# Kernel tuning notes

Hardware: AMD Instinct MI355X
Metric: run time of the kernel (lower is better)

The kernel has to match this reference:

```python
import jax, jax.numpy as jnp
import numpy as np


def _safe_pow(v, p):
    # mimic torch.nan_to_num(pow(v, p), nan=0, posinf=0, neginf=0) for v >= 0
    out = jnp.where(v > 0, jnp.power(jnp.where(v > 0, v, 1.0), p), 0.0)
    return out.astype(jnp.float32)


def setup_inputs() -> dict:
    key = jax.random.key(0)
    k1, k2, k3 = jax.random.split(key, 3)
    N, E, Din, Dout = 20000, 4096, 128, 128
    x = jax.random.normal(k1, (N, Din), dtype=jnp.float32)
    H = jax.random.uniform(k2, (N, E), dtype=jnp.float32)
    W = jax.random.normal(k3, (Dout, Din), dtype=jnp.float32) * (1.0 / np.sqrt(Din))
    b = jnp.zeros((Dout,), dtype=jnp.float32)
    return {"x": x, "H": H, "W": W, "b": b}


def reference(x, H, W, b):
    # Dv^{-1/2}: node degrees; De^{-1}: hyperedge degrees.
    # torch.diag(...)**p with nan/inf->0 is exactly diagonal scaling, so we
    # use broadcasted vector scaling fused around the two GEMMs.
    dv = _safe_pow(jnp.sum(H, axis=-1), -0.5)   # [N]
    de = _safe_pow(jnp.sum(H, axis=0), -1.0)    # [E]
    x = dv[:, None] * x                          # Dv^{-1/2} x
    x = H.T @ x                                  # [E, Din]
    x = de[:, None] * x                          # De^{-1}
    x = H @ x                                    # [N, Din]
    x = dv[:, None] * x                          # Dv^{-1/2}
    return x @ W.T + b                           # Linear
```

## Files before the change

kernel.cpp:

```cpp
#include <hip/hip_runtime.h>
#include <hip/hip_bf16.h>
#include <stdint.h>


#define N_ 20000
#define E_ 4096
#define D_ 128
#define XTB_S 20032
#define SPLIT 12

typedef __attribute__((ext_vector_type(8))) short    bf16x8;
typedef __attribute__((ext_vector_type(4))) float    f32x4;
typedef __attribute__((ext_vector_type(8))) unsigned short us8;
typedef __attribute__((ext_vector_type(4))) unsigned short us4;

__device__ __forceinline__ unsigned short f2bf(float f) {
  unsigned u = __float_as_uint(f);
  u += 0x7FFFu + ((u >> 16) & 1u);
  return (unsigned short)(u >> 16);
}
__device__ __forceinline__ unsigned cvtpk(float lo, float hi) {
  unsigned r;
  asm("v_cvt_pk_bf16_f32 %0, %1, %2" : "=v"(r) : "v"(lo), "v"(hi));
  return r;
}
__device__ __forceinline__ void gload16(const unsigned short* g, unsigned short* l) {
  __builtin_amdgcn_global_load_lds(
      (const __attribute__((address_space(1))) unsigned int*)g,
      (__attribute__((address_space(3))) unsigned int*)l, 16, 0, 0);
}

__global__ __launch_bounds__(256) void k_pre(const float* __restrict__ H,
                                             const float* __restrict__ x,
                                             const float* __restrict__ W,
                                             float* __restrict__ dv,
                                             unsigned short* __restrict__ Hb,
                                             unsigned short* __restrict__ xTb,
                                             unsigned short* __restrict__ Wb) {
  const int t = threadIdx.x, lane = t & 63, w = t >> 6;
  const int b = blockIdx.x;
  if (b >= 2500) {
    const size_t base = (size_t)(20000 + (b - 2500) * 8) * E_;
    for (int i = t; i < 4096; i += 256)
      *(us8*)&Hb[base + (size_t)i * 8] = (us8){0,0,0,0,0,0,0,0};
    if (b == 2500 && t < 128) {
#pragma unroll
      for (int c = 0; c < 4; ++c)
        *(us8*)&xTb[(size_t)t * XTB_S + 20000 + c * 8] = (us8){0,0,0,0,0,0,0,0};
    }
    if (b == 2501) {
      int base2 = t * 64;
#pragma unroll
      for (int i = 0; i < 8; ++i) {
        const float* wp = W + base2 + i * 8;
        f32x4 a = *(const f32x4*)wp, b4 = *(const f32x4*)(wp + 4);
        union { us8 v; unsigned u[4]; } un;
        un.u[0] = cvtpk(a.x, a.y);   un.u[1] = cvtpk(a.z, a.w);
        un.u[2] = cvtpk(b4.x, b4.y); un.u[3] = cvtpk(b4.z, b4.w);
        *(us8*)(Wb + base2 + i * 8) = un.v;
      }
    }
    return;
  }
  __shared__ float red[32];
  __shared__ float xt[8 * 128];
  const int n0 = b * 8;
  { int r = t >> 5, d4 = (t & 31) * 4;
    *(f32x4*)&xt[r * 128 + d4] = *(const f32x4*)(x + (size_t)(n0 + r) * D_ + d4); }
  float rs[8];
#pragma unroll
  for (int r = 0; r < 8; ++r) {
    rs[r] = 0.f;
    const float* rp = H + (size_t)(n0 + r) * E_;
    unsigned short* hp = Hb + (size_t)(n0 + r) * E_;
#pragma unroll
    for (int j = 0; j < 4; ++j) {
      f32x4 v = *(const f32x4*)(rp + j * 1024 + t * 4);
      rs[r] += (v.x + v.y) + (v.z + v.w);
      union { us4 v4; unsigned u32[2]; } un;
      un.u32[0] = cvtpk(v.x, v.y);
      un.u32[1] = cvtpk(v.z, v.w);
      *(us4*)(hp + j * 1024 + t * 4) = un.v4;
    }
  }
#pragma unroll
  for (int r = 0; r < 8; ++r)
#pragma unroll
    for (int off = 32; off; off >>= 1) rs[r] += __shfl_xor(rs[r], off);
  if (lane == 0) {
#pragma unroll
    for (int r = 0; r < 8; ++r) red[w * 8 + r] = rs[r];
  }
  __syncthreads();
  if (t < 8) {
    float s = red[t] + red[8 + t] + red[16 + t] + red[24 + t];
    float d = s > 0.f ? rsqrtf(s) : 0.f;
    dv[n0 + t] = d;
    red[t] = d;
  }
  __syncthreads();
  if (t < 128) {
    int d = t;
    float v[8];
#pragma unroll
    for (int r = 0; r < 8; ++r) v[r] = xt[r * 128 + d] * red[r];
    union { us8 v8; unsigned u32[4]; } un;
#pragma unroll
    for (int j = 0; j < 4; ++j) un.u32[j] = cvtpk(v[2 * j], v[2 * j + 1]);
    *(us8*)(xTb + (size_t)d * XTB_S + n0) = un.v8;
  }
}

__global__ __launch_bounds__(256) void k_gemm1(const unsigned short* __restrict__ Hb,
                                               const unsigned short* __restrict__ xTb,
                                               float* __restrict__ partialT,
                                               float* __restrict__ desumP) {
  __shared__ unsigned short lH[2][64 * 64];
  __shared__ unsigned short lX[2][128 * 64];
  const int t = threadIdx.x, lane = t & 63, w = t >> 6;
  const int virt = (blockIdx.x & 7) * 96 + (blockIdx.x >> 3);
  const int eb = virt & 63, s = virt >> 6;
  const int e0 = eb * 64;
  const int g0 = (s * 313) / SPLIT;
  const int g1 = ((s + 1) * 313) / SPLIT;
  const int lrow = lane >> 3, lslot = lane & 7;
  const int bswz = (lslot ^ lrow) << 3;
  const int wy = w >> 1, wx = w & 1;
  const int ep = t & 31, q = t >> 5;
  const int er0 = 2 * ep, er1 = 2 * ep + 1;
  const int sl0 = (q ^ (er0 & 7)) << 3, sl1 = (q ^ (er1 & 7)) << 3;

  f32x4 acc[4][2];
  f32x4 accC[2];
#pragma unroll
  for (int i = 0; i < 4; ++i)
#pragma unroll
    for (int j = 0; j < 2; ++j) acc[i][j] = (f32x4){0.f, 0.f, 0.f, 0.f};
  accC[0] = (f32x4){0.f, 0.f, 0.f, 0.f};
  accC[1] = (f32x4){0.f, 0.f, 0.f, 0.f};
  bf16x8 ones;
#pragma unroll
  for (int i = 0; i < 8; ++i) ones[i] = (short)0x3F80;

  unsigned hr[8];
  auto LOADH = [&](int g) {
    const unsigned short* p = Hb + (size_t)(g * 64 + q * 8) * E_ + e0 + er0;
#pragma unroll
    for (int j = 0; j < 8; ++j) hr[j] = *(const unsigned*)(p + (size_t)j * E_);
  };
  auto WRITEH = [&](int bufi) {
    union { bf16x8 v; unsigned u[4]; } lo, hi;
#pragma unroll
    for (int p = 0; p < 4; ++p) {
      lo.u[p] = (hr[2 * p] & 0xFFFFu) | (hr[2 * p + 1] << 16);
      hi.u[p] = (hr[2 * p] >> 16) | (hr[2 * p + 1] & 0xFFFF0000u);
    }
    *(bf16x8*)&lH[bufi][er0 * 64 + sl0] = lo.v;
    *(bf16x8*)&lH[bufi][er1 * 64 + sl1] = hi.v;
  };
  auto GLOADX = [&](int g, int bufi) {
#pragma unroll
    for (int i = 0; i < 4; ++i) {
      int c = w * 4 + i;
      gload16(xTb + (size_t)(8 * c + lrow) * XTB_S + g * 64 + bswz,
              &lX[bufi][c * 512]);
    }
  };

  LOADH(g0); GLOADX(g0, 0); WRITEH(0);
  __syncthreads();
  int cur = 0;
  for (int it = g0; it < g1; ++it) {
    bool hn = it + 1 < g1;
    if (hn) { LOADH(it + 1); GLOADX(it + 1, cur ^ 1); }
    const int kg = lane >> 4, fr = lane & 15;
    bf16x8 ax[4][2], bh[2][2];
#pragma unroll
    for (int mi = 0; mi < 4; ++mi) {
      int m = wy * 64 + mi * 16 + fr;
#pragma unroll
      for (int kk = 0; kk < 2; ++kk)
        ax[mi][kk] = *(const bf16x8*)&lX[cur][m * 64 + (((kk * 4 + kg) ^ (m & 7)) << 3)];
    }
#pragma unroll
    for (int ni = 0; ni < 2; ++ni) {
      int n = wx * 32 + ni * 16 + fr;
#pragma unroll
      for (int kk = 0; kk < 2; ++kk)
        bh[ni][kk] = *(const bf16x8*)&lH[cur][n * 64 + (((kk * 4 + kg) ^ (n & 7)) << 3)];
    }
#pragma unroll
    for (int kk = 0; kk < 2; ++kk)
#pragma unroll
      for (int mi = 0; mi < 4; ++mi)
#pragma unroll
        for (int ni = 0; ni < 2; ++ni)
          acc[mi][ni] = __builtin_amdgcn_mfma_f32_16x16x32_bf16(ax[mi][kk], bh[ni][kk], acc[mi][ni], 0, 0, 0);
    if (wy == 0) {
#pragma unroll
      for (int kk = 0; kk < 2; ++kk)
#pragma unroll
        for (int ni = 0; ni < 2; ++ni)
          accC[ni] = __builtin_amdgcn_mfma_f32_16x16x32_bf16(ones, bh[ni][kk], accC[ni], 0, 0, 0);
    }
    if (hn) WRITEH(cur ^ 1);
    __syncthreads();
    cur ^= 1;
  }
  const int kg = lane >> 4, fr = lane & 15;
  if (wy == 0 && kg == 0) {
#pragma unroll
    for (int ni = 0; ni < 2; ++ni)
      desumP[s * E_ + e0 + wx * 32 + ni * 16 + fr] = accC[ni][0];
  }
#pragma unroll
  for (int mi = 0; mi < 4; ++mi)
#pragma unroll
    for (int ni = 0; ni < 2; ++ni)
#pragma unroll
      for (int r = 0; r < 4; ++r) {
        int d = wy * 64 + mi * 16 + kg * 4 + r;
        int e = e0 + wx * 32 + ni * 16 + fr;
        partialT[((size_t)s * 128 + d) * E_ + e] = acc[mi][ni][r];
      }
}

__global__ __launch_bounds__(256) void k_mid(const float* __restrict__ partialT,
                                             const float* __restrict__ desumP,
                                             const unsigned short* __restrict__ Wb,
                                             unsigned short* __restrict__ x3WT) {
  __shared__ unsigned short lW[128 * 136];
  __shared__ unsigned short lE[16 * 132];
  __shared__ float lT[128 * 20];
  const int t = threadIdx.x, lane = t & 63, w = t >> 6;
  const int e0 = blockIdx.x * 16;

  {
    int j = t >> 1, half = (t & 1) * 64;
    const us8* src = (const us8*)(Wb + (size_t)j * 128 + half);
#pragma unroll
    for (int i = 0; i < 8; ++i)
      *(us8*)&lW[j * 136 + half + 8 * i] = src[i];
  }
  {
    const int e = e0 + (t & 15);
    const int d0 = (t >> 4) * 8;
    float des = 0.f;
#pragma unroll
    for (int s = 0; s < SPLIT; ++s) des += desumP[s * E_ + e];
    float dei = des > 0.f ? 1.f / des : 0.f;
    float accp[8];
#pragma unroll
    for (int i = 0; i < 8; ++i) accp[i] = 0.f;
#pragma unroll
    for (int s = 0; s < SPLIT; ++s) {
      const float* p = partialT + ((size_t)s * 128 + d0) * E_ + e;
#pragma unroll
      for (int i = 0; i < 8; ++i) accp[i] += p[(size_t)i * E_];
    }
    union { bf16x8 v; unsigned u[4]; } un;
#pragma unroll
    for (int i = 0; i < 4; ++i)
      un.u[i] = cvtpk(accp[2 * i] * dei, accp[2 * i + 1] * dei);
    *(bf16x8*)&lE[(t & 15) * 132 + d0] = un.v;
  }
  __syncthreads();
  const int kg = lane >> 4, fr = lane & 15;
  f32x4 acc[2];
  acc[0] = (f32x4){0.f, 0.f, 0.f, 0.f};
  acc[1] = (f32x4){0.f, 0.f, 0.f, 0.f};
#pragma unroll
  for (int kk = 0; kk < 4; ++kk) {
    bf16x8 bfrag = *(const bf16x8*)&lE[fr * 132 + (kk * 4 + kg) * 8];
#pragma unroll
    for (int mi = 0; mi < 2; ++mi) {
      int m = w * 32 + mi * 16 + fr;
      bf16x8 afrag = *(const bf16x8*)&lW[m * 136 + (kk * 4 + kg) * 8];
      acc[mi] = __builtin_amdgcn_mfma_f32_16x16x32_bf16(afrag, bfrag, acc[mi], 0, 0, 0);
    }
  }
  __syncthreads();
#pragma unroll
  for (int mi = 0; mi < 2; ++mi)
#pragma unroll
    for (int r = 0; r < 4; ++r)
      lT[(w * 32 + mi * 16 + kg * 4 + r) * 20 + fr] = acc[mi][r];
  __syncthreads();
  {
    int j = t >> 1, eh = (t & 1) * 8;
    float v[8];
#pragma unroll
    for (int i = 0; i < 8; ++i) v[i] = lT[j * 20 + eh + i];
    union { us8 v8; unsigned u[4]; } un;
#pragma unroll
    for (int i = 0; i < 4; ++i) un.u[i] = cvtpk(v[2 * i], v[2 * i + 1]);
    *(us8*)(x3WT + (size_t)j * E_ + e0 + eh) = un.v8;
  }
}

__global__ __launch_bounds__(256) void k_gemm2(const unsigned short* __restrict__ Hb,
                                               const unsigned short* __restrict__ x3WT,
                                               float* __restrict__ P) {
  __shared__ unsigned short lA[2][64 * 64];
  __shared__ unsigned short lB[2][128 * 64];
  const int t = threadIdx.x, lane = t & 63, w = t >> 6;
  const int tile = blockIdx.x >> 1, half = blockIdx.x & 1;
  const int n0b = tile * 64;
  const int gbase = half * 32;
  const int lrow = lane >> 3, lslot = lane & 7;
  const int bswz = (lslot ^ lrow) << 3;
  const int wy = w >> 1, wx = w & 1;

  auto GLOADA = [&](int g, int bufi) {
#pragma unroll
    for (int i = 0; i < 2; ++i) {
      int c = w * 2 + i;
      gload16(Hb + (size_t)(n0b + 8 * c + lrow) * E_ + g * 64 + bswz,
              &lA[bufi][c * 512]);
    }
  };
  auto GLOADB = [&](int g, int bufi) {
#pragma unroll
    for (int i = 0; i < 4; ++i) {
      int c = w * 4 + i;
      gload16(x3WT + (size_t)(8 * c + lrow) * E_ + g * 64 + bswz,
              &lB[bufi][c * 512]);
    }
  };

  f32x4 acc[2][4];
#pragma unroll
  for (int i = 0; i < 2; ++i)
#pragma unroll
    for (int j = 0; j < 4; ++j) acc[i][j] = (f32x4){0.f, 0.f, 0.f, 0.f};

  GLOADA(gbase, 0); GLOADB(gbase, 0);
  __syncthreads();
  int cur = 0;
  for (int it = 0; it < 32; ++it) {
    bool hn = it < 31;
    if (hn) { GLOADA(gbase + it + 1, cur ^ 1); GLOADB(gbase + it + 1, cur ^ 1); }
    const int kg = lane >> 4, fr = lane & 15;
    bf16x8 af[2][2], bfr[4][2];
#pragma unroll
    for (int mi = 0; mi < 2; ++mi) {
      int m = wy * 32 + mi * 16 + fr;
#pragma unroll
      for (int kk = 0; kk < 2; ++kk)
        af[mi][kk] = *(const bf16x8*)&lA[cur][m * 64 + (((kk * 4 + kg) ^ (m & 7)) << 3)];
    }
#pragma unroll
    for (int ni = 0; ni < 4; ++ni) {
      int d = wx * 64 + ni * 16 + fr;
#pragma unroll
      for (int kk = 0; kk < 2; ++kk)
        bfr[ni][kk] = *(const bf16x8*)&lB[cur][d * 64 + (((kk * 4 + kg) ^ (d & 7)) << 3)];
    }
#pragma unroll
    for (int kk = 0; kk < 2; ++kk)
#pragma unroll
      for (int mi = 0; mi < 2; ++mi)
#pragma unroll
        for (int ni = 0; ni < 4; ++ni)
          acc[mi][ni] = __builtin_amdgcn_mfma_f32_16x16x32_bf16(af[mi][kk], bfr[ni][kk], acc[mi][ni], 0, 0, 0);
    __syncthreads();
    cur ^= 1;
  }
  const int kg = lane >> 4, fr = lane & 15;
  float* Ph = P + (size_t)half * N_ * D_;
#pragma unroll
  for (int mi = 0; mi < 2; ++mi)
#pragma unroll
    for (int ni = 0; ni < 4; ++ni) {
      int j2 = wx * 64 + ni * 16 + fr;
#pragma unroll
      for (int r = 0; r < 4; ++r) {
        int n = n0b + wy * 32 + mi * 16 + kg * 4 + r;
        if (n < N_) Ph[(size_t)n * D_ + j2] = acc[mi][ni][r];
      }
    }
}

__global__ __launch_bounds__(256) void k_out(const float* __restrict__ P,
                                             const float* __restrict__ dv,
                                             const float* __restrict__ bias,
                                             float* __restrict__ out) {
  int tid = blockIdx.x * 256 + threadIdx.x;
  int n = tid >> 4, jb = (tid & 15) * 8;
  size_t off = (size_t)n * D_ + jb;
  f32x4 p0a = *(const f32x4*)(P + off);
  f32x4 p0b = *(const f32x4*)(P + off + 4);
  f32x4 p1a = *(const f32x4*)(P + (size_t)N_ * D_ + off);
  f32x4 p1b = *(const f32x4*)(P + (size_t)N_ * D_ + off + 4);
  f32x4 ba  = *(const f32x4*)(bias + jb);
  f32x4 bb  = *(const f32x4*)(bias + jb + 4);
  float d = dv[n];
  f32x4 oa = (p0a + p1a) * d + ba;
  f32x4 ob = (p0b + p1b) * d + bb;
  *(f32x4*)(out + off)     = oa;
  *(f32x4*)(out + off + 4) = ob;
}

extern "C" void kernel_launch(void* const* d_in, const int* in_sizes, int n_in,
                              void* d_out, int out_size, void* d_ws, size_t ws_size,
                              hipStream_t stream) {
  const float* x = (const float*)d_in[0];
  const float* H = (const float*)d_in[1];
  const float* W = (const float*)d_in[2];
  const float* b = (const float*)d_in[3];
  float* out = (float*)d_out;
  char* ws = (char*)d_ws;
  float*          desumP   = (float*)(ws);
  float*          dv       = (float*)(ws + 196608);
  unsigned short* Wb       = (unsigned short*)(ws + 276736);
  unsigned short* xTb      = (unsigned short*)(ws + 309504);
  unsigned short* x3WT     = (unsigned short*)(ws + 5437696);
  float*          partialT = (float*)(ws + 6486272);
  unsigned short* Hb       = (unsigned short*)(ws + 31652096);
  float*          P        = (float*)(ws + 195754240);

  k_pre<<<2504, 256, 0, stream>>>(H, x, W, dv, Hb, xTb, Wb);
  k_gemm1<<<768, 256, 0, stream>>>(Hb, xTb, partialT, desumP);
  k_mid<<<256, 256, 0, stream>>>(partialT, desumP, Wb, x3WT);
  k_gemm2<<<626, 256, 0, stream>>>(Hb, x3WT, P);
  k_out<<<1250, 256, 0, stream>>>(P, dv, b, out);
}
```

Baseline: 213.7 us.

## Deepen H register prefetch to two stages with explicit waitcnt and barriers

Turns the first GEMM's main loop into a two-stage register pipeline for H tiles. Two register sets alternate so the global load for tile it+2 is issued while tile it+1 is written to LDS and tile it is computed. The __syncthreads calls are replaced by explicit vmcnt/lgkmcnt waits and raw barriers, and the MFMA block is wrapped in s_setprio, all to hide global load latency behind compute. In exchange it uses more registers and relies on hand-counted waitcnt values that must match the number of outstanding loads.

```diff
diff --git a/kernel.cpp b/kernel.cpp
--- a/kernel.cpp
+++ b/kernel.cpp
@@ -29,6 +29,9 @@
       (const __attribute__((address_space(1))) unsigned int*)g,
       (__attribute__((address_space(3))) unsigned int*)l, 16, 0, 0);
 }
+#define VMCNT(n) asm volatile("s_waitcnt vmcnt(" #n ")" ::: "memory")
+#define LGKM0()  asm volatile("s_waitcnt lgkmcnt(0)" ::: "memory")
+#define BAR()    do { __builtin_amdgcn_s_barrier(); __builtin_amdgcn_sched_barrier(0); } while (0)
 
 __global__ __launch_bounds__(256) void k_pre(const float* __restrict__ H,
                                              const float* __restrict__ x,
@@ -142,13 +145,13 @@
 #pragma unroll
   for (int i = 0; i < 8; ++i) ones[i] = (short)0x3F80;
 
-  unsigned hr[8];
-  auto LOADH = [&](int g) {
+  unsigned hrA[8], hrB[8];
+  auto LOADH = [&](int g, unsigned (&hr)[8]) {
     const unsigned short* p = Hb + (size_t)(g * 64 + q * 8) * E_ + e0 + er0;
 #pragma unroll
     for (int j = 0; j < 8; ++j) hr[j] = *(const unsigned*)(p + (size_t)j * E_);
   };
-  auto WRITEH = [&](int bufi) {
+  auto WRITEH = [&](unsigned (&hr)[8], int bufi) {
     union { bf16x8 v; unsigned u[4]; } lo, hi;
 #pragma unroll
     for (int p = 0; p < 4; ++p) {
@@ -167,12 +170,10 @@
     }
   };
 
-  LOADH(g0); GLOADX(g0, 0); WRITEH(0);
-  __syncthreads();
-  int cur = 0;
-  for (int it = g0; it < g1; ++it) {
-    bool hn = it + 1 < g1;
-    if (hn) { LOADH(it + 1); GLOADX(it + 1, cur ^ 1); }
+  auto STEP = [&](int it, unsigned (&ld)[8], unsigned (&wr)[8], int par) {
+    const bool hn = it + 1 < g1;
+    if (hn) GLOADX(it + 1, par ^ 1);
+    { int g2 = (it + 2 < g1) ? it + 2 : g1 - 1; LOADH(g2, ld); }
     const int kg = lane >> 4, fr = lane & 15;
     bf16x8 ax[4][2], bh[2][2];
 #pragma unroll
@@ -180,15 +181,16 @@
       int m = wy * 64 + mi * 16 + fr;
 #pragma unroll
       for (int kk = 0; kk < 2; ++kk)
-        ax[mi][kk] = *(const bf16x8*)&lX[cur][m * 64 + (((kk * 4 + kg) ^ (m & 7)) << 3)];
+        ax[mi][kk] = *(const bf16x8*)&lX[par][m * 64 + (((kk * 4 + kg) ^ (m & 7)) << 3)];
     }
 #pragma unroll
     for (int ni = 0; ni < 2; ++ni) {
       int n = wx * 32 + ni * 16 + fr;
 #pragma unroll
       for (int kk = 0; kk < 2; ++kk)
-        bh[ni][kk] = *(const bf16x8*)&lH[cur][n * 64 + (((kk * 4 + kg) ^ (n & 7)) << 3)];
-    }
+        bh[ni][kk] = *(const bf16x8*)&lH[par][n * 64 + (((kk * 4 + kg) ^ (n & 7)) << 3)];
+    }
+    __builtin_amdgcn_s_setprio(1);
 #pragma unroll
     for (int kk = 0; kk < 2; ++kk)
 #pragma unroll
@@ -203,10 +205,28 @@
         for (int ni = 0; ni < 2; ++ni)
           accC[ni] = __builtin_amdgcn_mfma_f32_16x16x32_bf16(ones, bh[ni][kk], accC[ni], 0, 0, 0);
     }
-    if (hn) WRITEH(cur ^ 1);
-    __syncthreads();
-    cur ^= 1;
-  }
+    __builtin_amdgcn_s_setprio(0);
+    __builtin_amdgcn_sched_barrier(0);
+    if (hn) WRITEH(wr, par ^ 1);
+    VMCNT(8);
+    LGKM0();
+    BAR();
+  };
+
+  LOADH(g0, hrA);
+  GLOADX(g0, 0);
+  LOADH(g0 + 1, hrB);
+  WRITEH(hrA, 0);
+  VMCNT(8);
+  LGKM0();
+  BAR();
+
+  int it = g0;
+  while (it < g1) {
+    STEP(it, hrA, hrB, 0); ++it;
+    if (it < g1) { STEP(it, hrB, hrA, 1); ++it; }
+  }
+
   const int kg = lane >> 4, fr = lane & 15;
   if (wy == 0 && kg == 0) {
 #pragma unroll
```

After: 224.5 us. 1.05x slower.

## Drop LDS staging in gemm2; load MFMA fragments directly from global memory

Applied to the files above, without the earlier changes.

Rewrites the second GEMM kernel so each wave computes a 16-row by 128-column tile and reads its A and B MFMA fragments straight from global memory, removing the LDS double buffer and the block-wide barriers. The goal is to cut LDS traffic and synchronisation overhead. In exchange, B (x3WT) is re-read from global/L2 by every wave with no sharing through LDS. Per-lane 16-byte loads are strided across rows, which may give poorer coalescing and more pressure on L2 bandwidth.

```diff
diff --git a/kernel.cpp b/kernel.cpp
--- a/kernel.cpp
+++ b/kernel.cpp
@@ -301,84 +301,40 @@
 __global__ __launch_bounds__(256) void k_gemm2(const unsigned short* __restrict__ Hb,
                                                const unsigned short* __restrict__ x3WT,
                                                float* __restrict__ P) {
-  __shared__ unsigned short lA[2][64 * 64];
-  __shared__ unsigned short lB[2][128 * 64];
   const int t = threadIdx.x, lane = t & 63, w = t >> 6;
   const int tile = blockIdx.x >> 1, half = blockIdx.x & 1;
-  const int n0b = tile * 64;
-  const int gbase = half * 32;
-  const int lrow = lane >> 3, lslot = lane & 7;
-  const int bswz = (lslot ^ lrow) << 3;
-  const int wy = w >> 1, wx = w & 1;
-
-  auto GLOADA = [&](int g, int bufi) {
-#pragma unroll
-    for (int i = 0; i < 2; ++i) {
-      int c = w * 2 + i;
-      gload16(Hb + (size_t)(n0b + 8 * c + lrow) * E_ + g * 64 + bswz,
-              &lA[bufi][c * 512]);
-    }
-  };
-  auto GLOADB = [&](int g, int bufi) {
-#pragma unroll
-    for (int i = 0; i < 4; ++i) {
-      int c = w * 4 + i;
-      gload16(x3WT + (size_t)(8 * c + lrow) * E_ + g * 64 + bswz,
-              &lB[bufi][c * 512]);
-    }
-  };
-
-  f32x4 acc[2][4];
-#pragma unroll
-  for (int i = 0; i < 2; ++i)
-#pragma unroll
-    for (int j = 0; j < 4; ++j) acc[i][j] = (f32x4){0.f, 0.f, 0.f, 0.f};
-
-  GLOADA(gbase, 0); GLOADB(gbase, 0);
-  __syncthreads();
-  int cur = 0;
-  for (int it = 0; it < 32; ++it) {
-    bool hn = it < 31;
-    if (hn) { GLOADA(gbase + it + 1, cur ^ 1); GLOADB(gbase + it + 1, cur ^ 1); }
-    const int kg = lane >> 4, fr = lane & 15;
-    bf16x8 af[2][2], bfr[4][2];
-#pragma unroll
-    for (int mi = 0; mi < 2; ++mi) {
-      int m = wy * 32 + mi * 16 + fr;
-#pragma unroll
-      for (int kk = 0; kk < 2; ++kk)
-        af[mi][kk] = *(const bf16x8*)&lA[cur][m * 64 + (((kk * 4 + kg) ^ (m & 7)) << 3)];
-    }
-#pragma unroll
-    for (int ni = 0; ni < 4; ++ni) {
-      int d = wx * 64 + ni * 16 + fr;
-#pragma unroll
-      for (int kk = 0; kk < 2; ++kk)
-        bfr[ni][kk] = *(const bf16x8*)&lB[cur][d * 64 + (((kk * 4 + kg) ^ (d & 7)) << 3)];
-    }
-#pragma unroll
-    for (int kk = 0; kk < 2; ++kk)
-#pragma unroll
-      for (int mi = 0; mi < 2; ++mi)
-#pragma unroll
-        for (int ni = 0; ni < 4; ++ni)
-          acc[mi][ni] = __builtin_amdgcn_mfma_f32_16x16x32_bf16(af[mi][kk], bfr[ni][kk], acc[mi][ni], 0, 0, 0);
-    __syncthreads();
-    cur ^= 1;
-  }
-  const int kg = lane >> 4, fr = lane & 15;
+  const int n0w = tile * 64 + w * 16;
+  const int fr = lane & 15, kg = lane >> 4;
+  const int koff = half * 2048;
+
+  const unsigned short* Abase = Hb  + (size_t)(n0w + fr) * E_ + koff + kg * 8;
+  const unsigned short* Bbase = x3WT + (size_t)fr * E_        + koff + kg * 8;
+
+  f32x4 acc[8];
+#pragma unroll
+  for (int i = 0; i < 8; ++i) acc[i] = (f32x4){0.f, 0.f, 0.f, 0.f};
+
+#pragma unroll 4
+  for (int g = 0; g < 64; ++g) {
+    const bf16x8 a = *(const bf16x8*)(Abase + g * 32);
+    bf16x8 bfr[8];
+#pragma unroll
+    for (int ni = 0; ni < 8; ++ni)
+      bfr[ni] = *(const bf16x8*)(Bbase + (size_t)ni * 16 * E_ + g * 32);
+#pragma unroll
+    for (int ni = 0; ni < 8; ++ni)
+      acc[ni] = __builtin_amdgcn_mfma_f32_16x16x32_bf16(a, bfr[ni], acc[ni], 0, 0, 0);
+  }
   float* Ph = P + (size_t)half * N_ * D_;
 #pragma unroll
-  for (int mi = 0; mi < 2; ++mi)
-#pragma unroll
-    for (int ni = 0; ni < 4; ++ni) {
-      int j2 = wx * 64 + ni * 16 + fr;
-#pragma unroll
-      for (int r = 0; r < 4; ++r) {
-        int n = n0b + wy * 32 + mi * 16 + kg * 4 + r;
-        if (n < N_) Ph[(size_t)n * D_ + j2] = acc[mi][ni][r];
-      }
-    }
+  for (int ni = 0; ni < 8; ++ni) {
+    int j2 = ni * 16 + fr;
+#pragma unroll
+    for (int r = 0; r < 4; ++r) {
+      int n = n0w + kg * 4 + r;
+      if (n < N_) Ph[(size_t)n * D_ + j2] = acc[ni][r];
+    }
+  }
 }
 
 __global__ __launch_bounds__(256) void k_out(const float* __restrict__ P,
```

After: 365.6 us. +71.1%, slower.
